# Kernel optimization log

Measured on AMD Instinct MI355X. Metric: run time of the kernel, lower is better.

The kernel has to match this reference:

```python
import jax, jax.numpy as jnp
import numpy as np

DECAY = 0.99
EPS = 1e-05


def setup_inputs() -> dict:
    key = jax.random.key(0)
    k1, k2, k3 = jax.random.split(key, 3)
    inp = jax.random.normal(k1, (8, 1024, 512), dtype=jnp.float32)
    embed = jax.random.normal(k2, (512, 8192), dtype=jnp.float32)
    # buffers: cluster_size starts at zeros, embed_avg is a clone of embed in torch
    cluster_size = jnp.zeros((8192,), dtype=jnp.float32)
    embed_avg = embed
    return {"input": inp, "embed": embed, "cluster_size": cluster_size, "embed_avg": embed_avg}


def reference(input, embed, cluster_size, embed_avg):
    dim, n_embed = embed.shape
    flatten = input.reshape(-1, dim)  # [N, dim]
    # squared euclidean distance via expansion: ||f||^2 - 2 f.E + ||E||^2 -> [N, n_embed]
    dist = ((flatten ** 2).sum(axis=1, keepdims=True)
            - 2.0 * flatten @ embed
            + (embed ** 2).sum(axis=0, keepdims=True))
    embed_ind_flat = jnp.argmin(dist, axis=1)  # argmax of -dist == argmin of dist
    embed_ind = embed_ind_flat.reshape(input.shape[:-1])
    # nearest-codebook lookup: F.embedding(ind, embed.T)
    quantize = jnp.take(embed.T, embed_ind, axis=0)  # [..., dim]
    # training-mode EMA statistics (one-hot scatter sums, done without a dense one-hot)
    onehot_sum = jnp.zeros((n_embed,), flatten.dtype).at[embed_ind_flat].add(1.0)
    embed_sum = jax.ops.segment_sum(flatten, embed_ind_flat, num_segments=n_embed).T  # [dim, n_embed]
    new_cluster_size = cluster_size * DECAY + (1.0 - DECAY) * onehot_sum
    new_embed_avg = embed_avg * DECAY + (1.0 - DECAY) * embed_sum
    n = new_cluster_size.sum()
    cs = (new_cluster_size + EPS) / (n + n_embed * EPS) * n
    new_embed = new_embed_avg / cs[None, :]
    # commitment loss (quantize detached) and straight-through estimator
    diff = jnp.mean((jax.lax.stop_gradient(quantize) - input) ** 2)
    quantize_st = input + jax.lax.stop_gradient(quantize - input)
    return (quantize_st, diff, embed_ind, new_embed, new_cluster_size, new_embed_avg)
```

## Files before the change

### kernel.cpp

```cpp
#include <hip/hip_runtime.h>


constexpr int N = 8192;
constexpr int K = 512;
constexpr int M = 8192;

typedef unsigned short ushortT;
typedef __attribute__((ext_vector_type(8))) short s8v;
typedef __attribute__((ext_vector_type(4))) float f4v;

__device__ __forceinline__ ushortT f2bf(float x) {
    unsigned u = __float_as_uint(x);
    unsigned r = (u + 0x7FFFu + ((u >> 16) & 1u)) >> 16;
    return (ushortT)r;
}
__device__ __forceinline__ float bf2f(ushortT h) {
    return __uint_as_float(((unsigned)h) << 16);
}

typedef const __attribute__((address_space(1))) unsigned gau;
typedef __attribute__((address_space(3))) unsigned lau;
__device__ __forceinline__ void gl16(const void* g, void* l) {
    __builtin_amdgcn_global_load_lds((gau*)g, (lau*)l, 16, 0, 0);
}

__device__ __forceinline__ unsigned packDI(float d, int col) {
    unsigned u = __float_as_uint(d);
    unsigned s = (u & 0x80000000u) ? ~u : (u | 0x80000000u);
    return (s & ~0x1FFFu) | (unsigned)col;
}
__device__ __forceinline__ float unpackD(unsigned p) {
    unsigned s = p & ~0x1FFFu;
    unsigned u = (s & 0x80000000u) ? (s & 0x7fffffffu) : ~s;
    return __uint_as_float(u);
}
__device__ __forceinline__ void top2u(unsigned& a, unsigned& b, unsigned c) {
    unsigned mn = c < a ? c : a;
    unsigned mx = c < a ? a : c;
    a = mn;
    b = mx < b ? mx : b;
}

__global__ __launch_bounds__(256) void k_prep(
    const float* __restrict__ f, const float* __restrict__ E,
    ushortT* __restrict__ Fh, ushortT* __restrict__ EhT, ushortT* __restrict__ ElT,
    float* __restrict__ pc, float* __restrict__ counts) {
    __shared__ float tile[64][65];
    int b = blockIdx.x, t = threadIdx.x;
    if (b < 2048) {
        if (b < 32) counts[b * 256 + t] = 0.f;
        size_t i8 = ((size_t)b * 256 + t) * 8;
        float4 x0 = *(const float4*)&f[i8];
        float4 x1 = *(const float4*)&f[i8 + 4];
        float xs[8] = {x0.x, x0.y, x0.z, x0.w, x1.x, x1.y, x1.z, x1.w};
        union { s8v v; ushortT u[8]; } h;
#pragma unroll
        for (int j = 0; j < 8; ++j) h.u[j] = f2bf(xs[j]);
        *(s8v*)&Fh[i8] = h.v;
    } else {
        int bb = b - 2048;
        int jb = bb & 127, kb = bb >> 7;
        int jj = t & 63, kk0 = t >> 6;
        int j0 = jb * 64, k0 = kb * 64;
#pragma unroll
        for (int it = 0; it < 16; ++it) {
            int kk = it * 4 + kk0;
            tile[kk][jj] = E[(size_t)(k0 + kk) * M + j0 + jj];
        }
        __syncthreads();
        int r = t >> 2, ks = (t & 3) * 16;
        union { s8v v[2]; ushortT u[16]; } h, lo;
        float nrm = 0.f;
#pragma unroll
        for (int i = 0; i < 16; ++i) {
            float x = tile[ks + i][r];
            nrm = fmaf(x, x, nrm);
            ushortT hh = f2bf(x);
            h.u[i] = hh;
            lo.u[i] = f2bf(x - bf2f(hh));
        }
        size_t o = (size_t)(j0 + r) * K + k0 + ks;
        *(s8v*)&EhT[o] = h.v[0];
        *(s8v*)&EhT[o + 8] = h.v[1];
        *(s8v*)&ElT[o] = lo.v[0];
        *(s8v*)&ElT[o + 8] = lo.v[1];
        nrm += __shfl_down(nrm, 2);
        nrm += __shfl_down(nrm, 1);
        if ((t & 3) == 0) pc[(size_t)kb * M + j0 + r] = nrm;
    }
}

__global__ __launch_bounds__(512) void k_score(
    const ushortT* __restrict__ Fh, const ushortT* __restrict__ Eh,
    const float* __restrict__ pc, unsigned* __restrict__ pv) {
    __shared__ alignas(16) ushortT ls[2][2][256 * 64];

    int bid = blockIdx.x;
    int xcd = bid & 7, local = bid >> 3;
    int rb = xcd * 4 + (local & 3);
    int cb = local >> 2;
    int rowBase = rb * 256, colBase = cb * 256;
    int tid = threadIdx.x;
    int w = tid >> 6, l = tid & 63;
    int wr = w >> 2, wc = w & 3;
    int l15 = l & 15, g4 = l >> 4;
    int s7 = l15 & 7;

    const ushortT* srcA = Fh + (size_t)(rowBase + w * 32) * K;
    const ushortT* srcB = Eh + (size_t)(colBase + w * 32) * K;

    f4v acc[8][4];
#pragma unroll
    for (int m = 0; m < 8; ++m)
#pragma unroll
        for (int n = 0; n < 4; ++n) acc[m][n] = (f4v){0.f, 0.f, 0.f, 0.f};

#define STAGE(p, ch)                                                  \
    do {                                                              \
        _Pragma("unroll")                                             \
        for (int i_ = 0; i_ < 4; ++i_) {                              \
            int q_ = i_ * 64 + l;                                     \
            int row_ = q_ >> 3, slot_ = q_ & 7;                       \
            int swz_ = (slot_ ^ (row_ & 7)) * 8;                      \
            size_t so_ = (size_t)row_ * K + (ch) * 64 + swz_;         \
            gl16(srcA + so_, &ls[p][0][w * 2048 + q_ * 8]);           \
            gl16(srcB + so_, &ls[p][1][w * 2048 + q_ * 8]);           \
        }                                                             \
    } while (0)

    STAGE(0, 0);
    __syncthreads();

#pragma unroll
    for (int ch = 0; ch < 8; ++ch) {
        int p = ch & 1;
        if (ch < 7) STAGE(p ^ 1, ch + 1);
#pragma unroll
        for (int kk = 0; kk < 2; ++kk) {
            s8v a[8], b[4];
#pragma unroll
            for (int m = 0; m < 8; ++m) {
                int rA = wr * 128 + m * 16 + l15;
                a[m] = *(const s8v*)&ls[p][0][rA * 64 + ((kk * 4 + g4) ^ s7) * 8];
            }
#pragma unroll
            for (int n = 0; n < 4; ++n) {
                int rB = wc * 64 + n * 16 + l15;
                b[n] = *(const s8v*)&ls[p][1][rB * 64 + ((kk * 4 + g4) ^ s7) * 8];
            }
#pragma unroll
            for (int m = 0; m < 8; ++m)
#pragma unroll
                for (int n = 0; n < 4; ++n)
                    acc[m][n] = __builtin_amdgcn_mfma_f32_16x16x32_bf16(
                        a[m], b[n], acc[m][n], 0, 0, 0);
        }
        __syncthreads();
    }
#undef STAGE

    float cj[4];
#pragma unroll
    for (int n = 0; n < 4; ++n) {
        int col = colBase + wc * 64 + n * 16 + l15;
        float s = 0.f;
#pragma unroll
        for (int kb = 0; kb < 8; ++kb) s += pc[(size_t)kb * M + col];
        cj[n] = s;
    }
    unsigned* cand = (unsigned*)ls;

#pragma unroll
    for (int m = 0; m < 8; ++m)
#pragma unroll
        for (int q = 0; q < 4; ++q) {
            unsigned p0 = packDI(fmaf(-2.f, acc[m][0][q], cj[0]), colBase + wc * 64 + l15);
            unsigned p1 = packDI(fmaf(-2.f, acc[m][1][q], cj[1]), colBase + wc * 64 + 16 + l15);
            unsigned p2 = packDI(fmaf(-2.f, acc[m][2][q], cj[2]), colBase + wc * 64 + 32 + l15);
            unsigned p3 = packDI(fmaf(-2.f, acc[m][3][q], cj[3]), colBase + wc * 64 + 48 + l15);
            unsigned a_ = p0 < p1 ? p0 : p1;
            unsigned b_ = p0 < p1 ? p1 : p0;
            top2u(a_, b_, p2);
            top2u(a_, b_, p3);
#pragma unroll
            for (int mk = 8; mk >= 2; mk >>= 1) {
                unsigned oa = __shfl_xor((int)a_, mk);
                unsigned ob = __shfl_xor((int)b_, mk);
                top2u(a_, b_, oa);
                top2u(a_, b_, ob);
            }
            if (l15 < 2) {
                int row = wr * 128 + m * 16 + g4 * 4 + q;
                int slot = wc * 4 + l15 * 2;
                cand[row * 17 + slot] = a_;
                cand[row * 17 + slot + 1] = b_;
            }
        }
    __syncthreads();
    if (tid < 256) {
        unsigned best = cand[tid * 17], second = cand[tid * 17 + 1];
#pragma unroll
        for (int i = 2; i < 16; i += 2) {
            top2u(best, second, cand[tid * 17 + i]);
            top2u(best, second, cand[tid * 17 + i + 1]);
        }
        size_t o = (size_t)(rowBase + tid) * 64 + cb * 2;
        pv[o] = best;
        pv[o + 1] = second;
    }
}

__global__ __launch_bounds__(256) void k_combine(
    const unsigned* __restrict__ pv, const float* __restrict__ f,
    const ushortT* __restrict__ EhT, const ushortT* __restrict__ ElT,
    const float* __restrict__ pc,
    int* __restrict__ indws, float* __restrict__ o_ind, float* __restrict__ counts,
    float* __restrict__ o_q, float* __restrict__ diffp) {
    __shared__ float dsum[4];
    int w = threadIdx.x >> 6, l = threadIdx.x & 63;
    int row = blockIdx.x * 4 + w;
    unsigned e = pv[(size_t)row * 64 + l];
    unsigned mn = e;
#pragma unroll
    for (int m = 1; m < 64; m <<= 1) {
        unsigned o = __shfl_xor((int)mn, m);
        mn = o < mn ? o : mn;
    }
    float thr = unpackD(mn) + 2.0f;
    float dl = unpackD(e);
    float bestd = 3.4e38f; int bestj = 0x7fffffff;
    float4 fa = *(const float4*)&f[(size_t)row * K + l * 8];
    float4 fb = *(const float4*)&f[(size_t)row * K + l * 8 + 4];
    float fx[8] = {fa.x, fa.y, fa.z, fa.w, fb.x, fb.y, fb.z, fb.w};
    s8v qh, ql;
    unsigned long long mask = __ballot(dl <= thr);
    while (mask) {
        int b = __ffsll(mask) - 1;
        mask &= mask - 1;
        int j = (int)(__shfl((int)e, b) & 0x1fff);
        s8v hv = *(const s8v*)(EhT + (size_t)j * K + l * 8);
        s8v lv = *(const s8v*)(ElT + (size_t)j * K + l * 8);
        float a = 0.f;
#pragma unroll
        for (int q = 0; q < 8; ++q)
            a = fmaf(fx[q], bf2f((ushortT)hv[q]) + bf2f((ushortT)lv[q]), a);
#pragma unroll
        for (int m = 1; m < 64; m <<= 1) a += __shfl_xor(a, m);
        float cj = 0.f;
#pragma unroll
        for (int kb = 0; kb < 8; ++kb) cj += pc[(size_t)kb * M + j];
        float d = cj - 2.f * a;
        if (d < bestd || (d == bestd && j < bestj)) {
            bestd = d; bestj = j; qh = hv; ql = lv;
        }
    }
    float os[8];
    float local = 0.f;
#pragma unroll
    for (int q = 0; q < 8; ++q) {
        float qv = bf2f((ushortT)qh[q]) + bf2f((ushortT)ql[q]);
        float d = qv - fx[q];
        os[q] = fx[q] + d;
        local = fmaf(d, d, local);
    }
    float4 o0 = {os[0], os[1], os[2], os[3]};
    float4 o1 = {os[4], os[5], os[6], os[7]};
    *(float4*)&o_q[(size_t)row * K + l * 8] = o0;
    *(float4*)&o_q[(size_t)row * K + l * 8 + 4] = o1;
#pragma unroll
    for (int m = 1; m < 64; m <<= 1) local += __shfl_xor(local, m);
    if (l == 0) {
        indws[row] = bestj;
        o_ind[row] = (float)bestj;
        atomicAdd(&counts[bestj], 1.0f);
        dsum[w] = local;
    }
    __syncthreads();
    if (threadIdx.x == 0)
        diffp[blockIdx.x] = dsum[0] + dsum[1] + dsum[2] + dsum[3];
}

__global__ __launch_bounds__(256) void k_ema(
    const float* __restrict__ f, const int* __restrict__ indws,
    const float* __restrict__ ea, float* __restrict__ o_avg, float* __restrict__ o_ne,
    const float* __restrict__ cs_in, const float* __restrict__ counts,
    float* __restrict__ o_ncs,
    const float* __restrict__ diffp, float* __restrict__ o_diff) {
    int b = blockIdx.x, t = threadIdx.x;
    __shared__ float wsum[4];
    if (b == 256) {
        float loc = 0.f;
#pragma unroll 32
        for (int i = 0; i < 32; ++i) {
            int j = i * 256 + t;
            o_ncs[j] = 0.99f * cs_in[j] + 0.01f * counts[j];
        }
        float dl = 0.f;
#pragma unroll
        for (int i = 0; i < 8; ++i) dl += diffp[i * 256 + t];
#pragma unroll
        for (int off = 32; off; off >>= 1) dl += __shfl_down(dl, off);
        if ((t & 63) == 0) wsum[t >> 6] = dl;
        __syncthreads();
        if (t == 0)
            o_diff[0] = (wsum[0] + wsum[1] + wsum[2] + wsum[3]) * (1.0f / 4194304.0f);
        (void)loc;
        return;
    }
    __shared__ float acc[512 * 33];
    __shared__ int q[8192];
    __shared__ int qn;
    __shared__ float csr_s[32];
    __shared__ float nsh;
    for (int i = t; i < 512 * 33; i += 256) acc[i] = 0.f;
    if (t == 0) qn = 0;
    __syncthreads();
    for (int r = t; r < N; r += 256) {
        int j = indws[r];
        if ((j >> 5) == b) {
            int s = atomicAdd(&qn, 1);
            q[s] = (r << 5) | (j & 31);
        }
    }
    __syncthreads();
    int nq = qn;
    int s = 0;
    for (; s + 4 <= nq; s += 4) {
        int e0 = q[s], e1 = q[s + 1], e2 = q[s + 2], e3 = q[s + 3];
        float a0 = f[(size_t)(e0 >> 5) * K + t],       c0 = f[(size_t)(e0 >> 5) * K + t + 256];
        float a1 = f[(size_t)(e1 >> 5) * K + t],       c1 = f[(size_t)(e1 >> 5) * K + t + 256];
        float a2 = f[(size_t)(e2 >> 5) * K + t],       c2 = f[(size_t)(e2 >> 5) * K + t + 256];
        float a3 = f[(size_t)(e3 >> 5) * K + t],       c3 = f[(size_t)(e3 >> 5) * K + t + 256];
        acc[t * 33 + (e0 & 31)] += a0;         acc[(t + 256) * 33 + (e0 & 31)] += c0;
        acc[t * 33 + (e1 & 31)] += a1;         acc[(t + 256) * 33 + (e1 & 31)] += c1;
        acc[t * 33 + (e2 & 31)] += a2;         acc[(t + 256) * 33 + (e2 & 31)] += c2;
        acc[t * 33 + (e3 & 31)] += a3;         acc[(t + 256) * 33 + (e3 & 31)] += c3;
    }
    for (; s < nq; ++s) {
        int e = q[s];
        float a0 = f[(size_t)(e >> 5) * K + t];
        float c0 = f[(size_t)(e >> 5) * K + t + 256];
        acc[t * 33 + (e & 31)] += a0;
        acc[(t + 256) * 33 + (e & 31)] += c0;
    }
    float loc = 0.f;
#pragma unroll 32
    for (int i = 0; i < 32; ++i) {
        int j = i * 256 + t;
        loc += 0.99f * cs_in[j] + 0.01f * counts[j];
    }
#pragma unroll
    for (int off = 32; off; off >>= 1) loc += __shfl_down(loc, off);
    __syncthreads();
    if ((t & 63) == 0) wsum[t >> 6] = loc;
    __syncthreads();
    if (t == 0) nsh = wsum[0] + wsum[1] + wsum[2] + wsum[3];
    __syncthreads();
    if (t < 32) {
        int j = b * 32 + t;
        float v = 0.99f * cs_in[j] + 0.01f * counts[j];
        float n = nsh;
        csr_s[t] = (v + 1e-5f) / (n + 8192.0f * 1e-5f) * n;
    }
    __syncthreads();
    for (int i = t; i < 512 * 32; i += 256) {
        int d = i >> 5, c = i & 31;
        size_t o = (size_t)d * M + b * 32 + c;
        float val = 0.99f * ea[o] + 0.01f * acc[d * 33 + c];
        o_avg[o] = val;
        o_ne[o] = val / csr_s[c];
    }
}

extern "C" void kernel_launch(void* const* d_in, const int* in_sizes, int n_in,
                              void* d_out, int out_size, void* d_ws, size_t ws_size,
                              hipStream_t stream) {
    const float* f     = (const float*)d_in[0];
    const float* E     = (const float*)d_in[1];
    const float* cs_in = (const float*)d_in[2];
    const float* ea    = (const float*)d_in[3];

    float* out = (float*)d_out;
    float* o_q    = out;
    float* o_diff = out + 4194304;
    float* o_ind  = out + 4194305;
    float* o_ne   = out + 4202497;
    float* o_ncs  = out + 8396801;
    float* o_avg  = out + 8404993;

    ushortT* Fh  = (ushortT*)o_q;
    ushortT* EhT = (ushortT*)o_ne;
    ushortT* ElT = EhT + (size_t)M * K;
    unsigned* pv = (unsigned*)o_avg;

    float* wsf    = (float*)d_ws;
    float* counts = wsf + 8192;
    int*   indws  = (int*)(wsf + 24576);
    float* diffp  = wsf + 32768;
    float* pc     = wsf + 40960;

    k_prep   <<<3072, 256, 0, stream>>>(f, E, Fh, EhT, ElT, pc, counts);
    k_score  <<<1024, 512, 0, stream>>>(Fh, EhT, pc, pv);
    k_combine<<<2048, 256, 0, stream>>>(pv, f, EhT, ElT, pc, indws, o_ind, counts,
                                        o_q, diffp);
    k_ema    <<<257, 256, 0, stream>>>(f, indws, ea, o_avg, o_ne,
                                       cs_in, counts, o_ncs,
                                       diffp, o_diff);
}
```

Measured before the change: 161.0 us.

## Restructure GEMM main loop into quadrant-wise LDS reads interleaved with MFMA and barriers

Rewrites the distance GEMM inner loop so that two K-chunks are prefetched up front, with vmcnt waits replacing the full __syncthreads. The A and B fragments are read in halves and interleaved with MFMA quadrants, each group bracketed by s_barrier and lgkmcnt waits and raised wave priority (setprio) during MFMA bursts. The goal is to overlap LDS reads and global-to-LDS loads with matrix math and to cut register pressure from holding all fragments at once. It adds many barriers and hand-placed waitcnts, which may serialize the waves or be fragile if the counts are wrong.

Result: slower. 173.6 us (+7.8%).

```diff
diff --git a/kernel.cpp b/kernel.cpp
--- a/kernel.cpp
+++ b/kernel.cpp
@@ -128,36 +128,84 @@
         }                                                             \
     } while (0)
 
+#define READ_A(p, hh)                                                          \
+    do {                                                                       \
+        _Pragma("unroll")                                                      \
+        for (int m_ = 0; m_ < 4; ++m_)                                         \
+            _Pragma("unroll")                                                  \
+            for (int kk_ = 0; kk_ < 2; ++kk_)                                  \
+                a[m_][kk_] = *(const s8v*)&ls[p][0][                           \
+                    (wr * 128 + (hh) * 64 + m_ * 16 + l15) * 64 +              \
+                    ((kk_ * 4 + g4) ^ s7) * 8];                                \
+    } while (0)
+#define READ_B(p, nh)                                                          \
+    do {                                                                       \
+        _Pragma("unroll")                                                      \
+        for (int n_ = 0; n_ < 2; ++n_)                                         \
+            _Pragma("unroll")                                                  \
+            for (int kk_ = 0; kk_ < 2; ++kk_)                                  \
+                b[nh][n_][kk_] = *(const s8v*)&ls[p][1][                       \
+                    (wc * 64 + (nh) * 32 + n_ * 16 + l15) * 64 +               \
+                    ((kk_ * 4 + g4) ^ s7) * 8];                                \
+    } while (0)
+#define MFMA_Q(mh, nh)                                                         \
+    do {                                                                       \
+        __builtin_amdgcn_s_setprio(1);                                         \
+        _Pragma("unroll")                                                      \
+        for (int m_ = 0; m_ < 4; ++m_)                                         \
+            _Pragma("unroll")                                                  \
+            for (int n_ = 0; n_ < 2; ++n_)                                     \
+                _Pragma("unroll")                                              \
+                for (int kk_ = 0; kk_ < 2; ++kk_)                              \
+                    acc[(mh) * 4 + m_][(nh) * 2 + n_] =                        \
+                        __builtin_amdgcn_mfma_f32_16x16x32_bf16(               \
+                            a[m_][kk_], b[nh][n_][kk_],                        \
+                            acc[(mh) * 4 + m_][(nh) * 2 + n_], 0, 0, 0);       \
+        __builtin_amdgcn_s_setprio(0);                                         \
+    } while (0)
+#define LGKM0()                                                \
+    asm volatile("s_waitcnt lgkmcnt(0)" ::: "memory");         \
+    __builtin_amdgcn_sched_barrier(0)
+
     STAGE(0, 0);
-    __syncthreads();
-
-#pragma unroll
-    for (int ch = 0; ch < 8; ++ch) {
-        int p = ch & 1;
-        if (ch < 7) STAGE(p ^ 1, ch + 1);
-#pragma unroll
-        for (int kk = 0; kk < 2; ++kk) {
-            s8v a[8], b[4];
-#pragma unroll
-            for (int m = 0; m < 8; ++m) {
-                int rA = wr * 128 + m * 16 + l15;
-                a[m] = *(const s8v*)&ls[p][0][rA * 64 + ((kk * 4 + g4) ^ s7) * 8];
-            }
-#pragma unroll
-            for (int n = 0; n < 4; ++n) {
-                int rB = wc * 64 + n * 16 + l15;
-                b[n] = *(const s8v*)&ls[p][1][rB * 64 + ((kk * 4 + g4) ^ s7) * 8];
-            }
-#pragma unroll
-            for (int m = 0; m < 8; ++m)
-#pragma unroll
-                for (int n = 0; n < 4; ++n)
-                    acc[m][n] = __builtin_amdgcn_mfma_f32_16x16x32_bf16(
-                        a[m], b[n], acc[m][n], 0, 0, 0);
-        }
-        __syncthreads();
-    }
+    STAGE(1, 1);
+
+    s8v a[4][2], b[2][2][2];
+#pragma unroll 2
+    for (int kt = 0; kt < 8; ++kt) {
+        int p = kt & 1;
+        if (kt < 7) {
+            asm volatile("s_waitcnt vmcnt(8)" ::: "memory");
+        } else {
+            asm volatile("s_waitcnt vmcnt(0)" ::: "memory");
+        }
+        __builtin_amdgcn_s_barrier();
+        READ_A(p, 0);
+        READ_B(p, 0);
+        __builtin_amdgcn_s_barrier();
+        LGKM0();
+        MFMA_Q(0, 0);
+        __builtin_amdgcn_s_barrier();
+        READ_B(p, 1);
+        __builtin_amdgcn_s_barrier();
+        LGKM0();
+        MFMA_Q(0, 1);
+        __builtin_amdgcn_s_barrier();
+        READ_A(p, 1);
+        __builtin_amdgcn_s_barrier();
+        LGKM0();
+        MFMA_Q(1, 1);
+        __builtin_amdgcn_s_barrier();
+        MFMA_Q(1, 0);
+        __builtin_amdgcn_s_barrier();
+        if (kt < 6) STAGE(p, kt + 2);
+    }
+    __builtin_amdgcn_sched_barrier(0);
 #undef STAGE
+#undef READ_A
+#undef READ_B
+#undef MFMA_Q
+#undef LGKM0
 
     float cj[4];
 #pragma unroll
@@ -289,7 +337,6 @@
     int b = blockIdx.x, t = threadIdx.x;
     __shared__ float wsum[4];
     if (b == 256) {
-        float loc = 0.f;
 #pragma unroll 32
         for (int i = 0; i < 32; ++i) {
             int j = i * 256 + t;
@@ -304,7 +351,6 @@
         __syncthreads();
         if (t == 0)
             o_diff[0] = (wsum[0] + wsum[1] + wsum[2] + wsum[3]) * (1.0f / 4194304.0f);
-        (void)loc;
         return;
     }
     __shared__ float acc[512 * 33];
```

## Shrink score GEMM tiles to 128x128 with 32-wide K chunks

Applied to the files above, without the earlier changes.

The distance GEMM block tile shrinks from 256x256 (512 threads, 64-wide K chunks) to 128x128 (256 threads, 32-wide K chunks), with a new LDS swizzle and 4096 blocks. The candidate buffer per row doubles to 64 column blocks of top-2 entries, so the combine kernel now reads 128 candidates per row and rescans both slots. The aim is more blocks in flight and lower LDS and register use per block. The cost is less operand reuse per loaded byte, twice as many K-loop barriers, and more candidate traffic into the rescoring step.

Result: slower. 173.5 us (+7.8%).

```diff
diff --git a/kernel.cpp b/kernel.cpp
--- a/kernel.cpp
+++ b/kernel.cpp
@@ -90,71 +90,66 @@
     }
 }
 
-__global__ __launch_bounds__(512) void k_score(
+__global__ __launch_bounds__(256) void k_score(
     const ushortT* __restrict__ Fh, const ushortT* __restrict__ Eh,
     const float* __restrict__ pc, unsigned* __restrict__ pv) {
-    __shared__ alignas(16) ushortT ls[2][2][256 * 64];
+    __shared__ alignas(16) ushortT ls[2][2][128 * 32];
 
     int bid = blockIdx.x;
     int xcd = bid & 7, local = bid >> 3;
-    int rb = xcd * 4 + (local & 3);
-    int cb = local >> 2;
-    int rowBase = rb * 256, colBase = cb * 256;
+    int rb = xcd * 8 + (local & 7);
+    int cb = local >> 3;
+    int rowBase = rb * 128, colBase = cb * 128;
     int tid = threadIdx.x;
     int w = tid >> 6, l = tid & 63;
-    int wr = w >> 2, wc = w & 3;
+    int wr = w >> 1, wc = w & 1;
     int l15 = l & 15, g4 = l >> 4;
-    int s7 = l15 & 7;
-
-    const ushortT* srcA = Fh + (size_t)(rowBase + w * 32) * K;
-    const ushortT* srcB = Eh + (size_t)(colBase + w * 32) * K;
-
-    f4v acc[8][4];
-#pragma unroll
-    for (int m = 0; m < 8; ++m)
+
+    const ushortT* srcA = Fh + (size_t)rowBase * K;
+    const ushortT* srcB = Eh + (size_t)colBase * K;
+
+    f4v acc[4][4];
+#pragma unroll
+    for (int m = 0; m < 4; ++m)
 #pragma unroll
         for (int n = 0; n < 4; ++n) acc[m][n] = (f4v){0.f, 0.f, 0.f, 0.f};
 
 #define STAGE(p, ch)                                                  \
     do {                                                              \
         _Pragma("unroll")                                             \
-        for (int i_ = 0; i_ < 4; ++i_) {                              \
-            int q_ = i_ * 64 + l;                                     \
-            int row_ = q_ >> 3, slot_ = q_ & 7;                       \
-            int swz_ = (slot_ ^ (row_ & 7)) * 8;                      \
-            size_t so_ = (size_t)row_ * K + (ch) * 64 + swz_;         \
-            gl16(srcA + so_, &ls[p][0][w * 2048 + q_ * 8]);           \
-            gl16(srcB + so_, &ls[p][1][w * 2048 + q_ * 8]);           \
+        for (int i_ = 0; i_ < 2; ++i_) {                              \
+            int q_ = i_ * 256 + tid;                                  \
+            int row_ = q_ >> 2, slot_ = q_ & 3;                       \
+            int swz_ = (slot_ ^ ((row_ >> 1) & 3)) * 8;               \
+            size_t so_ = (size_t)row_ * K + (ch) * 32 + swz_;         \
+            gl16(srcA + so_, &ls[p][0][q_ * 8]);                      \
+            gl16(srcB + so_, &ls[p][1][q_ * 8]);                      \
         }                                                             \
     } while (0)
 
     STAGE(0, 0);
     __syncthreads();
 
-#pragma unroll
-    for (int ch = 0; ch < 8; ++ch) {
+    for (int ch = 0; ch < 16; ++ch) {
         int p = ch & 1;
-        if (ch < 7) STAGE(p ^ 1, ch + 1);
-#pragma unroll
-        for (int kk = 0; kk < 2; ++kk) {
-            s8v a[8], b[4];
-#pragma unroll
-            for (int m = 0; m < 8; ++m) {
-                int rA = wr * 128 + m * 16 + l15;
-                a[m] = *(const s8v*)&ls[p][0][rA * 64 + ((kk * 4 + g4) ^ s7) * 8];
-            }
-#pragma unroll
-            for (int n = 0; n < 4; ++n) {
-                int rB = wc * 64 + n * 16 + l15;
-                b[n] = *(const s8v*)&ls[p][1][rB * 64 + ((kk * 4 + g4) ^ s7) * 8];
-            }
-#pragma unroll
-            for (int m = 0; m < 8; ++m)
-#pragma unroll
-                for (int n = 0; n < 4; ++n)
-                    acc[m][n] = __builtin_amdgcn_mfma_f32_16x16x32_bf16(
-                        a[m], b[n], acc[m][n], 0, 0, 0);
-        }
+        if (ch < 15) STAGE(p ^ 1, ch + 1);
+        s8v a[4], b[4];
+#pragma unroll
+        for (int m = 0; m < 4; ++m) {
+            int rA = wr * 64 + m * 16 + l15;
+            a[m] = *(const s8v*)&ls[p][0][rA * 32 + ((g4 ^ ((rA >> 1) & 3)) * 8)];
+        }
+#pragma unroll
+        for (int n = 0; n < 4; ++n) {
+            int rB = wc * 64 + n * 16 + l15;
+            b[n] = *(const s8v*)&ls[p][1][rB * 32 + ((g4 ^ ((rB >> 1) & 3)) * 8)];
+        }
+#pragma unroll
+        for (int m = 0; m < 4; ++m)
+#pragma unroll
+            for (int n = 0; n < 4; ++n)
+                acc[m][n] = __builtin_amdgcn_mfma_f32_16x16x32_bf16(
+                    a[m], b[n], acc[m][n], 0, 0, 0);
         __syncthreads();
     }
 #undef STAGE
@@ -171,7 +166,7 @@
     unsigned* cand = (unsigned*)ls;
 
 #pragma unroll
-    for (int m = 0; m < 8; ++m)
+    for (int m = 0; m < 4; ++m)
 #pragma unroll
         for (int q = 0; q < 4; ++q) {
             unsigned p0 = packDI(fmaf(-2.f, acc[m][0][q], cj[0]), colBase + wc * 64 + l15);
@@ -190,21 +185,21 @@
                 top2u(a_, b_, ob);
             }
             if (l15 < 2) {
-                int row = wr * 128 + m * 16 + g4 * 4 + q;
+                int row = wr * 64 + m * 16 + g4 * 4 + q;
                 int slot = wc * 4 + l15 * 2;
-                cand[row * 17 + slot] = a_;
-                cand[row * 17 + slot + 1] = b_;
+                cand[row * 9 + slot] = a_;
+                cand[row * 9 + slot + 1] = b_;
             }
         }
     __syncthreads();
-    if (tid < 256) {
-        unsigned best = cand[tid * 17], second = cand[tid * 17 + 1];
-#pragma unroll
-        for (int i = 2; i < 16; i += 2) {
-            top2u(best, second, cand[tid * 17 + i]);
-            top2u(best, second, cand[tid * 17 + i + 1]);
-        }
-        size_t o = (size_t)(rowBase + tid) * 64 + cb * 2;
+    if (tid < 128) {
+        unsigned best = cand[tid * 9], second = cand[tid * 9 + 1];
+#pragma unroll
+        for (int i = 2; i < 8; i += 2) {
+            top2u(best, second, cand[tid * 9 + i]);
+            top2u(best, second, cand[tid * 9 + i + 1]);
+        }
+        size_t o = (size_t)(rowBase + tid) * 128 + cb * 2;
         pv[o] = best;
         pv[o + 1] = second;
     }
@@ -219,39 +214,43 @@
     __shared__ float dsum[4];
     int w = threadIdx.x >> 6, l = threadIdx.x & 63;
     int row = blockIdx.x * 4 + w;
-    unsigned e = pv[(size_t)row * 64 + l];
-    unsigned mn = e;
+    uint2 e2 = *(const uint2*)&pv[(size_t)row * 128 + l * 2];
+    unsigned mn = e2.x < e2.y ? e2.x : e2.y;
 #pragma unroll
     for (int m = 1; m < 64; m <<= 1) {
         unsigned o = __shfl_xor((int)mn, m);
         mn = o < mn ? o : mn;
     }
     float thr = unpackD(mn) + 2.0f;
-    float dl = unpackD(e);
     float bestd = 3.4e38f; int bestj = 0x7fffffff;
     float4 fa = *(const float4*)&f[(size_t)row * K + l * 8];
     float4 fb = *(const float4*)&f[(size_t)row * K + l * 8 + 4];
     float fx[8] = {fa.x, fa.y, fa.z, fa.w, fb.x, fb.y, fb.z, fb.w};
     s8v qh, ql;
-    unsigned long long mask = __ballot(dl <= thr);
-    while (mask) {
-        int b = __ffsll(mask) - 1;
-        mask &= mask - 1;
-        int j = (int)(__shfl((int)e, b) & 0x1fff);
-        s8v hv = *(const s8v*)(EhT + (size_t)j * K + l * 8);
-        s8v lv = *(const s8v*)(ElT + (size_t)j * K + l * 8);
-        float a = 0.f;
-#pragma unroll
-        for (int q = 0; q < 8; ++q)
-            a = fmaf(fx[q], bf2f((ushortT)hv[q]) + bf2f((ushortT)lv[q]), a);
-#pragma unroll
-        for (int m = 1; m < 64; m <<= 1) a += __shfl_xor(a, m);
-        float cj = 0.f;
-#pragma unroll
-        for (int kb = 0; kb < 8; ++kb) cj += pc[(size_t)kb * M + j];
-        float d = cj - 2.f * a;
-        if (d < bestd || (d == bestd && j < bestj)) {
-            bestd = d; bestj = j; qh = hv; ql = lv;
+#pragma unroll
+    for (int s = 0; s < 2; ++s) {
+        unsigned ev = s ? e2.y : e2.x;
+        float dl = unpackD(ev);
+        unsigned long long mask = __ballot(dl <= thr);
+        while (mask) {
+            int b = __ffsll(mask) - 1;
+            mask &= mask - 1;
+            int j = (int)(__shfl((int)ev, b) & 0x1fff);
+            s8v hv = *(const s8v*)(EhT + (size_t)j * K + l * 8);
+            s8v lv = *(const s8v*)(ElT + (size_t)j * K + l * 8);
+            float a = 0.f;
+#pragma unroll
+            for (int q = 0; q < 8; ++q)
+                a = fmaf(fx[q], bf2f((ushortT)hv[q]) + bf2f((ushortT)lv[q]), a);
+#pragma unroll
+            for (int m = 1; m < 64; m <<= 1) a += __shfl_xor(a, m);
+            float cj = 0.f;
+#pragma unroll
+            for (int kb = 0; kb < 8; ++kb) cj += pc[(size_t)kb * M + j];
+            float d = cj - 2.f * a;
+            if (d < bestd || (d == bestd && j < bestj)) {
+                bestd = d; bestj = j; qh = hv; ql = lv;
+            }
         }
     }
     float os[8];
@@ -289,7 +288,6 @@
     int b = blockIdx.x, t = threadIdx.x;
     __shared__ float wsum[4];
     if (b == 256) {
-        float loc = 0.f;
 #pragma unroll 32
         for (int i = 0; i < 32; ++i) {
             int j = i * 256 + t;
@@ -304,7 +302,6 @@
         __syncthreads();
         if (t == 0)
             o_diff[0] = (wsum[0] + wsum[1] + wsum[2] + wsum[3]) * (1.0f / 4194304.0f);
-        (void)loc;
         return;
     }
     __shared__ float acc[512 * 33];
@@ -400,7 +397,7 @@
     float* pc     = wsf + 40960;
 
     k_prep   <<<3072, 256, 0, stream>>>(f, E, Fh, EhT, ElT, pc, counts);
-    k_score  <<<1024, 512, 0, stream>>>(Fh, EhT, pc, pv);
+    k_score  <<<4096, 256, 0, stream>>>(Fh, EhT, pc, pv);
     k_combine<<<2048, 256, 0, stream>>>(pv, f, EhT, ElT, pc, indws, o_ind, counts,
                                         o_q, diffp);
     k_ema    <<<257, 256, 0, stream>>>(f, indws, ea, o_avg, o_ne,
```

## Deepen score GEMM pipeline to four LDS stages with 32-wide K chunks

Applied to the files above, without the earlier changes.

Restructures the k_score bf16 MFMA main loop from a two-buffer pipeline with 64-wide K chunks into a four-buffer pipeline with 32-wide chunks. It keeps three chunks of global-to-LDS loads in flight, using explicit vmcnt waits and raw barriers in place of __syncthreads. The LDS swizzle is redone for the narrower rows. The aim is to hide global load latency behind MFMA work, at the cost of more barriers, finer-grained loads and hand-tuned wait counts that must match the number of loads outstanding.

Measured after the change: 167.5 us. +4.1%, slower.

```diff
diff --git a/kernel.cpp b/kernel.cpp
--- a/kernel.cpp
+++ b/kernel.cpp
@@ -93,7 +93,7 @@
 __global__ __launch_bounds__(512) void k_score(
     const ushortT* __restrict__ Fh, const ushortT* __restrict__ Eh,
     const float* __restrict__ pc, unsigned* __restrict__ pv) {
-    __shared__ alignas(16) ushortT ls[2][2][256 * 64];
+    __shared__ alignas(16) ushortT ls[4][2][256 * 32];
 
     int bid = blockIdx.x;
     int xcd = bid & 7, local = bid >> 3;
@@ -104,7 +104,6 @@
     int w = tid >> 6, l = tid & 63;
     int wr = w >> 2, wc = w & 3;
     int l15 = l & 15, g4 = l >> 4;
-    int s7 = l15 & 7;
 
     const ushortT* srcA = Fh + (size_t)(rowBase + w * 32) * K;
     const ushortT* srcB = Eh + (size_t)(colBase + w * 32) * K;
@@ -118,45 +117,58 @@
 #define STAGE(p, ch)                                                  \
     do {                                                              \
         _Pragma("unroll")                                             \
-        for (int i_ = 0; i_ < 4; ++i_) {                              \
+        for (int i_ = 0; i_ < 2; ++i_) {                              \
             int q_ = i_ * 64 + l;                                     \
-            int row_ = q_ >> 3, slot_ = q_ & 7;                       \
-            int swz_ = (slot_ ^ (row_ & 7)) * 8;                      \
-            size_t so_ = (size_t)row_ * K + (ch) * 64 + swz_;         \
-            gl16(srcA + so_, &ls[p][0][w * 2048 + q_ * 8]);           \
-            gl16(srcB + so_, &ls[p][1][w * 2048 + q_ * 8]);           \
+            int row_ = q_ >> 2, slot_ = q_ & 3;                       \
+            int swz_ = (slot_ ^ ((row_ >> 1) & 3)) * 8;               \
+            size_t so_ = (size_t)row_ * K + (ch) * 32 + swz_;         \
+            gl16(srcA + so_, &ls[p][0][w * 1024 + q_ * 8]);           \
+            gl16(srcB + so_, &ls[p][1][w * 1024 + q_ * 8]);           \
         }                                                             \
     } while (0)
 
+#define BODY(p)                                                                \
+    do {                                                                       \
+        s8v a[8], b[4];                                                        \
+        _Pragma("unroll")                                                      \
+        for (int m_ = 0; m_ < 8; ++m_) {                                       \
+            int rA = wr * 128 + m_ * 16 + l15;                                 \
+            a[m_] = *(const s8v*)&ls[p][0][rA * 32 +                           \
+                                           ((g4 ^ ((rA >> 1) & 3)) * 8)];      \
+        }                                                                      \
+        _Pragma("unroll")                                                      \
+        for (int n_ = 0; n_ < 4; ++n_) {                                       \
+            int rB = wc * 64 + n_ * 16 + l15;                                  \
+            b[n_] = *(const s8v*)&ls[p][1][rB * 32 +                           \
+                                           ((g4 ^ ((rB >> 1) & 3)) * 8)];      \
+        }                                                                      \
+        _Pragma("unroll")                                                      \
+        for (int m_ = 0; m_ < 8; ++m_)                                         \
+            _Pragma("unroll")                                                  \
+            for (int n_ = 0; n_ < 4; ++n_)                                     \
+                acc[m_][n_] = __builtin_amdgcn_mfma_f32_16x16x32_bf16(         \
+                    a[m_], b[n_], acc[m_][n_], 0, 0, 0);                       \
+    } while (0)
+
+#define CHUNK(ch, vm)                                                 \
+    do {                                                              \
+        asm volatile("s_waitcnt vmcnt(" #vm ")" ::: "memory");        \
+        __builtin_amdgcn_s_barrier();                                 \
+        __builtin_amdgcn_sched_barrier(0);                            \
+        if ((ch) + 3 < 16) STAGE(((ch) + 3) & 3, (ch) + 3);           \
+        BODY((ch) & 3);                                               \
+    } while (0)
+
     STAGE(0, 0);
-    __syncthreads();
-
-#pragma unroll
-    for (int ch = 0; ch < 8; ++ch) {
-        int p = ch & 1;
-        if (ch < 7) STAGE(p ^ 1, ch + 1);
-#pragma unroll
-        for (int kk = 0; kk < 2; ++kk) {
-            s8v a[8], b[4];
-#pragma unroll
-            for (int m = 0; m < 8; ++m) {
-                int rA = wr * 128 + m * 16 + l15;
-                a[m] = *(const s8v*)&ls[p][0][rA * 64 + ((kk * 4 + g4) ^ s7) * 8];
-            }
-#pragma unroll
-            for (int n = 0; n < 4; ++n) {
-                int rB = wc * 64 + n * 16 + l15;
-                b[n] = *(const s8v*)&ls[p][1][rB * 64 + ((kk * 4 + g4) ^ s7) * 8];
-            }
-#pragma unroll
-            for (int m = 0; m < 8; ++m)
-#pragma unroll
-                for (int n = 0; n < 4; ++n)
-                    acc[m][n] = __builtin_amdgcn_mfma_f32_16x16x32_bf16(
-                        a[m], b[n], acc[m][n], 0, 0, 0);
-        }
-        __syncthreads();
-    }
+    STAGE(1, 1);
+    STAGE(2, 2);
+
+    CHUNK(0, 8);   CHUNK(1, 8);   CHUNK(2, 8);   CHUNK(3, 8);
+    CHUNK(4, 8);   CHUNK(5, 8);   CHUNK(6, 8);   CHUNK(7, 8);
+    CHUNK(8, 8);   CHUNK(9, 8);   CHUNK(10, 8);  CHUNK(11, 8);
+    CHUNK(12, 8);  CHUNK(13, 8);  CHUNK(14, 4);  CHUNK(15, 0);
+#undef CHUNK
+#undef BODY
 #undef STAGE
 
     float cj[4];
@@ -289,7 +301,6 @@
     int b = blockIdx.x, t = threadIdx.x;
     __shared__ float wsum[4];
     if (b == 256) {
-        float loc = 0.f;
 #pragma unroll 32
         for (int i = 0; i < 32; ++i) {
             int j = i * 256 + t;
@@ -304,7 +315,6 @@
         __syncthreads();
         if (t == 0)
             o_diff[0] = (wsum[0] + wsum[1] + wsum[2] + wsum[3]) * (1.0f / 4194304.0f);
-        (void)loc;
         return;
     }
     __shared__ float acc[512 * 33];
```
